# Performance work log

Measured on AMD Instinct MI355X. Metric: run time of the kernel, lower is better.

Reference implementation:

```python
import jax, jax.numpy as jnp
import numpy as np

WIN = 1024
HOP = 256

def setup_inputs() -> dict:
    key = jax.random.key(0)
    x = jax.random.normal(key, (16, WIN, 2048), dtype=jnp.float32)
    return {"x": x}

def reference(x) -> jnp.ndarray:
    # Overlap-add: y[b, f*hop + c] += x[b, c, f]
    B, win, n_frames = x.shape
    hop = HOP
    out_len = (n_frames - 1) * hop + win
    idx = jnp.arange(win)[:, None] + hop * jnp.arange(n_frames)[None, :]
    y = jnp.zeros((B, out_len), dtype=x.dtype)
    y = y.at[:, idx].add(x)
    return y
```

## Files before the change

### kernel.cpp

```cpp
#include <hip/hip_runtime.h>


constexpr int BATCH   = 16;
constexpr int WIN     = 1024;
constexpr int HOP     = 256;
constexpr int NF      = 2048;
constexpr int OUT_LEN = (NF - 1) * HOP + WIN;
constexpr int GTOT    = OUT_LEN / HOP;
constexpr int FT      = 128;
constexpr int NTILES  = (GTOT + FT - 1) / FT;
constexpr int RB      = 32;
constexpr int NRS     = HOP / RB;
constexpr int RS2     = FT + 4;

typedef float f4u __attribute__((ext_vector_type(4), aligned(4)));
typedef float f4a __attribute__((ext_vector_type(4), aligned(16)));

__global__ __launch_bounds__(256, 8)
void oadd_kernel(const float* __restrict__ x, float* __restrict__ y) {
    __shared__ __align__(16) float accT2[RB][RS2];

    const int tid   = threadIdx.x;
    const int tile  = blockIdx.x;
    const int rsp   = blockIdx.y;
    const int b     = blockIdx.z;
    const int g0    = tile * FT;
    const int rbase = rsp * RB;

    const int lane = tid & 63;
    const int w    = tid >> 6;
    const int fq   = (lane & 31) * 4;
    const int rh   = lane >> 5;

    const float* __restrict__ xb = x + (size_t)b * WIN * NF;

    const bool interior = (g0 >= 3) && (g0 + FT - 1 <= NF - 1);

    if (interior) {
        #pragma unroll
        for (int ip = 0; ip < 2; ++ip) {
            f4u v[2][4];
            #pragma unroll
            for (int i2 = 0; i2 < 2; ++i2) {
                const int it = ip * 2 + i2;
                const int rl = it * 8 + w * 2 + rh;
                const float* rp = xb + (size_t)(rbase + rl) * NF + (g0 + fq);
                #pragma unroll
                for (int k = 0; k < 4; ++k) {
                    v[i2][k] = *reinterpret_cast<const f4u*>(rp + (size_t)(k * HOP) * NF - k);
                }
            }
            #pragma unroll
            for (int i2 = 0; i2 < 2; ++i2) {
                const int it = ip * 2 + i2;
                const int rl = it * 8 + w * 2 + rh;
                f4u s = (v[i2][0] + v[i2][1]) + (v[i2][2] + v[i2][3]);
                *reinterpret_cast<f4a*>(&accT2[rl][fq]) = s;
            }
        }
    } else {
        #pragma unroll
        for (int it = 0; it < 4; ++it) {
            const int rl = it * 8 + w * 2 + rh;
            const int r  = rbase + rl;
            float a[4] = {0.f, 0.f, 0.f, 0.f};
            #pragma unroll
            for (int k = 0; k < 4; ++k) {
                const float* rp = xb + (size_t)(k * HOP + r) * NF;
                const int f0 = g0 + fq - k;
                if (f0 >= 0 && f0 + 3 <= NF - 1) {
                    f4u vv = *reinterpret_cast<const f4u*>(rp + f0);
                    a[0] += vv.x; a[1] += vv.y; a[2] += vv.z; a[3] += vv.w;
                } else {
                    #pragma unroll
                    for (int m = 0; m < 4; ++m) {
                        const int f = f0 + m;
                        if (f >= 0 && f < NF) a[m] += rp[f];
                    }
                }
            }
            accT2[rl][fq + 0] = a[0];
            accT2[rl][fq + 1] = a[1];
            accT2[rl][fq + 2] = a[2];
            accT2[rl][fq + 3] = a[3];
        }
    }

    __syncthreads();

    float* __restrict__ yb = y + (size_t)b * OUT_LEN;
    const int c4 = (tid & 7) * 4;
    const int jj = tid >> 3;
    #pragma unroll
    for (int pass = 0; pass < 4; ++pass) {
        const int j = pass * 32 + jj;
        const int g = g0 + j;
        if (g < GTOT) {
            f4a v;
            v.x = accT2[c4 + 0][j];
            v.y = accT2[c4 + 1][j];
            v.z = accT2[c4 + 2][j];
            v.w = accT2[c4 + 3][j];
            *reinterpret_cast<f4a*>(&yb[(size_t)g * HOP + rbase + c4]) = v;
        }
    }
}

extern "C" void kernel_launch(void* const* d_in, const int* in_sizes, int n_in,
                              void* d_out, int out_size, void* d_ws, size_t ws_size,
                              hipStream_t stream) {
    const float* x = (const float*)d_in[0];
    float* y = (float*)d_out;
    dim3 grid(NTILES, NRS, BATCH);
    oadd_kernel<<<grid, 256, 0, stream>>>(x, y);
}
```

Measured before the change: 41.88 us.

## Process two row slices per block with overlapped loads, LDS swizzle, nontemporal stores

Each block now handles two row slices (rbase and rbase+HOP/2) and issues the global loads for the second slice before writing out the first, so load latency overlaps with the transpose-and-store phase. LDS columns are XOR-swizzled by row to reduce bank conflicts on the transposed read, and output stores become nontemporal. This halves the grid size and adds extra barriers per block, which may reduce parallelism.

Result: slower. 49.81 us (+18.9%).

```diff
diff --git a/kernel.cpp b/kernel.cpp
--- a/kernel.cpp
+++ b/kernel.cpp
@@ -10,7 +10,7 @@
 constexpr int FT      = 128;
 constexpr int NTILES  = (GTOT + FT - 1) / FT;
 constexpr int RB      = 32;
-constexpr int NRS     = HOP / RB;
+constexpr int NPAIR   = HOP / RB / 2;
 constexpr int RS2     = FT + 4;
 
 typedef float f4u __attribute__((ext_vector_type(4), aligned(4)));
@@ -20,55 +20,73 @@
 void oadd_kernel(const float* __restrict__ x, float* __restrict__ y) {
     __shared__ __align__(16) float accT2[RB][RS2];
 
-    const int tid   = threadIdx.x;
-    const int tile  = blockIdx.x;
-    const int rsp   = blockIdx.y;
-    const int b     = blockIdx.z;
-    const int g0    = tile * FT;
-    const int rbase = rsp * RB;
+    const int tid  = threadIdx.x;
+    const int tile = blockIdx.x;
+    const int pr   = blockIdx.y;
+    const int b    = blockIdx.z;
+    const int g0   = tile * FT;
+    const int rbaseA = pr * RB;
+    const int rbaseB = rbaseA + (HOP / 2);
 
     const int lane = tid & 63;
     const int w    = tid >> 6;
     const int fq   = (lane & 31) * 4;
     const int rh   = lane >> 5;
+    const int rlw  = w * 2 + rh;
+
+    const int c4 = (tid & 7) * 4;
+    const int jj = tid >> 3;
 
     const float* __restrict__ xb = x + (size_t)b * WIN * NF;
+    float* __restrict__ yb = y + (size_t)b * OUT_LEN;
 
-    const bool interior = (g0 >= 3) && (g0 + FT - 1 <= NF - 1);
+    const bool interior = (g0 >= 3) && (g0 + FT <= NF);
 
-    if (interior) {
+    auto loadBatch = [&](int rbase, int ip, f4u (&v)[2][4]) {
         #pragma unroll
-        for (int ip = 0; ip < 2; ++ip) {
-            f4u v[2][4];
+        for (int i2 = 0; i2 < 2; ++i2) {
+            const int rl = (ip * 2 + i2) * 8 + rlw;
+            const float* rp = xb + (size_t)(rbase + rl) * NF + (g0 + fq);
             #pragma unroll
-            for (int i2 = 0; i2 < 2; ++i2) {
-                const int it = ip * 2 + i2;
-                const int rl = it * 8 + w * 2 + rh;
-                const float* rp = xb + (size_t)(rbase + rl) * NF + (g0 + fq);
-                #pragma unroll
-                for (int k = 0; k < 4; ++k) {
-                    v[i2][k] = *reinterpret_cast<const f4u*>(rp + (size_t)(k * HOP) * NF - k);
-                }
-            }
-            #pragma unroll
-            for (int i2 = 0; i2 < 2; ++i2) {
-                const int it = ip * 2 + i2;
-                const int rl = it * 8 + w * 2 + rh;
-                f4u s = (v[i2][0] + v[i2][1]) + (v[i2][2] + v[i2][3]);
-                *reinterpret_cast<f4a*>(&accT2[rl][fq]) = s;
+            for (int k = 0; k < 4; ++k)
+                v[i2][k] = *reinterpret_cast<const f4u*>(rp + (size_t)(k * HOP) * NF - k);
+        }
+    };
+    auto sumStore = [&](int ip, f4u (&v)[2][4]) {
+        #pragma unroll
+        for (int i2 = 0; i2 < 2; ++i2) {
+            const int rl = (ip * 2 + i2) * 8 + rlw;
+            f4u s = (v[i2][0] + v[i2][1]) + (v[i2][2] + v[i2][3]);
+            *reinterpret_cast<f4a*>(&accT2[rl][fq ^ (rl & 24)]) = s;
+        }
+    };
+    auto phase2 = [&](int rbase) {
+        #pragma unroll
+        for (int pass = 0; pass < 4; ++pass) {
+            const int j = pass * 32 + jj;
+            const int g = g0 + j;
+            if (g < GTOT) {
+                f4a v;
+                v.x = accT2[c4 + 0][j ^ ((c4 + 0) & 24)];
+                v.y = accT2[c4 + 1][j ^ ((c4 + 1) & 24)];
+                v.z = accT2[c4 + 2][j ^ ((c4 + 2) & 24)];
+                v.w = accT2[c4 + 3][j ^ ((c4 + 3) & 24)];
+                __builtin_nontemporal_store(
+                    v, reinterpret_cast<f4a*>(&yb[(size_t)g * HOP + rbase + c4]));
             }
         }
-    } else {
+    };
+    auto phase1Guarded = [&](int rbase) {
         #pragma unroll
         for (int it = 0; it < 4; ++it) {
-            const int rl = it * 8 + w * 2 + rh;
+            const int rl = it * 8 + rlw;
             const int r  = rbase + rl;
             float a[4] = {0.f, 0.f, 0.f, 0.f};
             #pragma unroll
             for (int k = 0; k < 4; ++k) {
                 const float* rp = xb + (size_t)(k * HOP + r) * NF;
                 const int f0 = g0 + fq - k;
-                if (f0 >= 0 && f0 + 3 <= NF - 1) {
+                if (f0 >= 0 && f0 + 3 < NF) {
                     f4u vv = *reinterpret_cast<const f4u*>(rp + f0);
                     a[0] += vv.x; a[1] += vv.y; a[2] += vv.z; a[3] += vv.w;
                 } else {
@@ -79,30 +97,38 @@
                     }
                 }
             }
-            accT2[rl][fq + 0] = a[0];
-            accT2[rl][fq + 1] = a[1];
-            accT2[rl][fq + 2] = a[2];
-            accT2[rl][fq + 3] = a[3];
+            const int base = fq ^ (rl & 24);
+            accT2[rl][base + 0] = a[0];
+            accT2[rl][base + 1] = a[1];
+            accT2[rl][base + 2] = a[2];
+            accT2[rl][base + 3] = a[3];
         }
-    }
+    };
 
-    __syncthreads();
-
-    float* __restrict__ yb = y + (size_t)b * OUT_LEN;
-    const int c4 = (tid & 7) * 4;
-    const int jj = tid >> 3;
-    #pragma unroll
-    for (int pass = 0; pass < 4; ++pass) {
-        const int j = pass * 32 + jj;
-        const int g = g0 + j;
-        if (g < GTOT) {
-            f4a v;
-            v.x = accT2[c4 + 0][j];
-            v.y = accT2[c4 + 1][j];
-            v.z = accT2[c4 + 2][j];
-            v.w = accT2[c4 + 3][j];
-            *reinterpret_cast<f4a*>(&yb[(size_t)g * HOP + rbase + c4]) = v;
+    if (interior) {
+        {
+            f4u v[2][4];
+            loadBatch(rbaseA, 0, v); sumStore(0, v);
+            loadBatch(rbaseA, 1, v); sumStore(1, v);
         }
+        __syncthreads();
+        f4u vb[2][4];
+        loadBatch(rbaseB, 0, vb);
+        phase2(rbaseA);
+        __syncthreads();
+        sumStore(0, vb);
+        loadBatch(rbaseB, 1, vb);
+        sumStore(1, vb);
+        __syncthreads();
+        phase2(rbaseB);
+    } else {
+        phase1Guarded(rbaseA);
+        __syncthreads();
+        phase2(rbaseA);
+        __syncthreads();
+        phase1Guarded(rbaseB);
+        __syncthreads();
+        phase2(rbaseB);
     }
 }
 
@@ -111,6 +137,6 @@
                               hipStream_t stream) {
     const float* x = (const float*)d_in[0];
     float* y = (float*)d_out;
-    dim3 grid(NTILES, NRS, BATCH);
+    dim3 grid(NTILES, NPAIR, BATCH);
     oadd_kernel<<<grid, 256, 0, stream>>>(x, y);
 }
```

## Stage input tiles into LDS via global_load_lds and sum during writeout

Applied to the files above, without the earlier changes.

The interior path now moves the four shifted input rows straight from global memory into LDS using the direct global-to-LDS load builtin, skipping the trip through registers. The four-way overlap sum is deferred to the transpose/writeout phase, where it reads all four LDS planes. This raises LDS use to 64KB per block and lowers the launch-bounds occupancy hint from 8 to 2. It also makes each wave issue 16-byte loads from unaligned addresses (g0+fq-k), which may not suit the LDS-direct load path and could break alignment or correctness.

After: 40.89 us. 2.4% less time.

```diff
diff --git a/kernel.cpp b/kernel.cpp
--- a/kernel.cpp
+++ b/kernel.cpp
@@ -11,14 +11,12 @@
 constexpr int NTILES  = (GTOT + FT - 1) / FT;
 constexpr int RB      = 32;
 constexpr int NRS     = HOP / RB;
-constexpr int RS2     = FT + 4;
 
-typedef float f4u __attribute__((ext_vector_type(4), aligned(4)));
 typedef float f4a __attribute__((ext_vector_type(4), aligned(16)));
 
-__global__ __launch_bounds__(256, 8)
+__global__ __launch_bounds__(256, 2)
 void oadd_kernel(const float* __restrict__ x, float* __restrict__ y) {
-    __shared__ __align__(16) float accT2[RB][RS2];
+    __shared__ float L[4][RB][FT];
 
     const int tid   = threadIdx.x;
     const int tile  = blockIdx.x;
@@ -34,74 +32,55 @@
 
     const float* __restrict__ xb = x + (size_t)b * WIN * NF;
 
-    const bool interior = (g0 >= 3) && (g0 + FT - 1 <= NF - 1);
+    const bool interior = (g0 >= 3) && (g0 + FT <= NF);
 
     if (interior) {
         #pragma unroll
-        for (int ip = 0; ip < 2; ++ip) {
-            f4u v[2][4];
+        for (int it = 0; it < 4; ++it) {
+            const int rl = it * 8 + w * 2;
             #pragma unroll
-            for (int i2 = 0; i2 < 2; ++i2) {
-                const int it = ip * 2 + i2;
-                const int rl = it * 8 + w * 2 + rh;
-                const float* rp = xb + (size_t)(rbase + rl) * NF + (g0 + fq);
-                #pragma unroll
-                for (int k = 0; k < 4; ++k) {
-                    v[i2][k] = *reinterpret_cast<const f4u*>(rp + (size_t)(k * HOP) * NF - k);
-                }
-            }
-            #pragma unroll
-            for (int i2 = 0; i2 < 2; ++i2) {
-                const int it = ip * 2 + i2;
-                const int rl = it * 8 + w * 2 + rh;
-                f4u s = (v[i2][0] + v[i2][1]) + (v[i2][2] + v[i2][3]);
-                *reinterpret_cast<f4a*>(&accT2[rl][fq]) = s;
+            for (int k = 0; k < 4; ++k) {
+                const float* src = xb + (size_t)(k * HOP + rbase + rl + rh) * NF
+                                      + (g0 + fq - k);
+                __builtin_amdgcn_global_load_lds(
+                    (const __attribute__((address_space(1))) unsigned int*)src,
+                    (__attribute__((address_space(3))) unsigned int*)&L[k][rl][0],
+                    16, 0, 0);
             }
         }
     } else {
         #pragma unroll
         for (int it = 0; it < 4; ++it) {
             const int rl = it * 8 + w * 2 + rh;
-            const int r  = rbase + rl;
-            float a[4] = {0.f, 0.f, 0.f, 0.f};
             #pragma unroll
             for (int k = 0; k < 4; ++k) {
-                const float* rp = xb + (size_t)(k * HOP + r) * NF;
-                const int f0 = g0 + fq - k;
-                if (f0 >= 0 && f0 + 3 <= NF - 1) {
-                    f4u vv = *reinterpret_cast<const f4u*>(rp + f0);
-                    a[0] += vv.x; a[1] += vv.y; a[2] += vv.z; a[3] += vv.w;
-                } else {
-                    #pragma unroll
-                    for (int m = 0; m < 4; ++m) {
-                        const int f = f0 + m;
-                        if (f >= 0 && f < NF) a[m] += rp[f];
-                    }
+                const float* rp = xb + (size_t)(k * HOP + rbase + rl) * NF;
+                #pragma unroll
+                for (int m = 0; m < 4; ++m) {
+                    const int f = g0 + fq + m - k;
+                    L[k][rl][fq + m] = (f >= 0 && f < NF) ? rp[f] : 0.f;
                 }
             }
-            accT2[rl][fq + 0] = a[0];
-            accT2[rl][fq + 1] = a[1];
-            accT2[rl][fq + 2] = a[2];
-            accT2[rl][fq + 3] = a[3];
         }
     }
 
     __syncthreads();
 
     float* __restrict__ yb = y + (size_t)b * OUT_LEN;
-    const int c4 = (tid & 7) * 4;
-    const int jj = tid >> 3;
+    const int jj = tid & 31;
+    const int rq = tid >> 5;
     #pragma unroll
-    for (int pass = 0; pass < 4; ++pass) {
-        const int j = pass * 32 + jj;
+    for (int p = 0; p < 4; ++p) {
+        const int j = p * 32 + jj;
         const int g = g0 + j;
         if (g < GTOT) {
             f4a v;
-            v.x = accT2[c4 + 0][j];
-            v.y = accT2[c4 + 1][j];
-            v.z = accT2[c4 + 2][j];
-            v.w = accT2[c4 + 3][j];
-            *reinterpret_cast<f4a*>(&yb[(size_t)g * HOP + rbase + c4]) = v;
+            #pragma unroll
+            for (int m = 0; m < 4; ++m) {
+                const int rl = rq * 4 + m;
+                v[m] = (L[0][rl][j] + L[1][rl][j]) + (L[2][rl][j] + L[3][rl][j]);
+            }
+            *reinterpret_cast<f4a*>(&yb[(size_t)g * HOP + rbase + rq * 4]) = v;
         }
     }
 }
```
